# Kernel optimization log

Hardware: AMD Instinct MI355X
Metric: run time of the kernel (lower is better)

## Reference

```python
import jax, jax.numpy as jnp
import numpy as np

B, T, D, V, MEM = 2, 512, 512, 256, 256


def _gru(x, h0, wih, whh, bih, bhh):
    # x: [B,T,D], h0: [B,D]; torch GRU gate order: r, z, n
    def step(h, xt):
        gi = xt @ wih.T + bih            # [B,3D]
        gh = h @ whh.T + bhh             # [B,3D]
        i_r, i_z, i_n = jnp.split(gi, 3, axis=-1)
        h_r, h_z, h_n = jnp.split(gh, 3, axis=-1)
        r = jax.nn.sigmoid(i_r + h_r)
        z = jax.nn.sigmoid(i_z + h_z)
        n = jnp.tanh(i_n + r * h_n)
        h_new = (1.0 - z) * n + z * h
        return h_new, h_new
    hT, ys = jax.lax.scan(step, h0, jnp.swapaxes(x, 0, 1))
    return jnp.swapaxes(ys, 0, 1), hT


def _layernorm(x, g, b, eps=1e-5):
    m = jnp.mean(x, axis=-1, keepdims=True)
    v = jnp.mean((x - m) ** 2, axis=-1, keepdims=True)
    return (x - m) / jnp.sqrt(v + eps) * g + b


def setup_inputs() -> dict:
    key = jax.random.key(0)
    ks = jax.random.split(key, 24)
    s = 1.0 / np.sqrt(D)
    inp = {
        'x': jax.random.randint(ks[0], (B, T), 0, V, dtype=jnp.int32),
        'h_f': jnp.zeros((1, B, D), jnp.float32),
        'h_s': jnp.zeros((1, B, D), jnp.float32),
        'soma_w': jax.random.normal(ks[1], (V, D), jnp.float32),
        'fast_wih': jax.random.normal(ks[2], (3 * D, D)) * s,
        'fast_whh': jax.random.normal(ks[3], (3 * D, D)) * s,
        'fast_bih': jax.random.normal(ks[4], (3 * D,)) * s,
        'fast_bhh': jax.random.normal(ks[5], (3 * D,)) * s,
        'slow_wih': jax.random.normal(ks[6], (3 * D, D)) * s,
        'slow_whh': jax.random.normal(ks[7], (3 * D, D)) * s,
        'slow_bih': jax.random.normal(ks[8], (3 * D,)) * s,
        'slow_bhh': jax.random.normal(ks[9], (3 * D,)) * s,
        'qkv_w': jax.random.normal(ks[10], (3 * D, D)) * s,
        'qkv_b': jax.random.normal(ks[11], (3 * D,)) * s,
        'gate_w': jax.random.normal(ks[12], (D, D)) * s,
        'gate_b': jax.random.normal(ks[13], (D,)) * s,
        'gate_g': jnp.ones((D,), jnp.float32),
        'gate_bb': jnp.zeros((D,), jnp.float32),
        'mem_bank': jax.random.normal(ks[14], (MEM, D)) * 0.1,
        'hip_qw': jax.random.normal(ks[15], (D, D)) * s,
        'hip_qb': jax.random.normal(ks[16], (D,)) * s,
        'axon_w': jax.random.normal(ks[17], (D, 4 * D)) * (0.5 * s),
        'axon_b': jax.random.normal(ks[18], (D,)) * s,
        'norm_g': jnp.ones((D,), jnp.float32),
        'norm_b': jnp.zeros((D,), jnp.float32),
    }
    return inp


def reference(x, h_f, h_s, soma_w, fast_wih, fast_whh, fast_bih, fast_bhh,
              slow_wih, slow_whh, slow_bih, slow_bhh, qkv_w, qkv_b,
              gate_w, gate_b, gate_g, gate_bb, mem_bank, hip_qw, hip_qb,
              axon_w, axon_b, norm_g, norm_b):
    d = soma_w.shape[1]
    s_in = soma_w[x]  # mod[0] == 1.0
    p_f, hf1 = _gru(s_in, h_f[0], fast_wih, fast_whh, fast_bih, fast_bhh)
    p_s, hs1 = _gru(p_f, h_s[0], slow_wih, slow_whh, slow_bih, slow_bhh)
    # LinearIntentMemory: naive cumulative outer-product linear attention
    qkv = p_s @ qkv_w.T + qkv_b
    q, k, v = jnp.split(qkv, 3, axis=-1)
    q = jax.nn.elu(q) + 1.0
    k = jax.nn.elu(k) + 1.0
    kv_cum = jnp.cumsum(jnp.einsum('bti,btj->btij', k, v), axis=1)  # [B,T,D,D]
    num = jnp.einsum('bti,btij->btj', q, kv_cum)
    den = jnp.einsum('bti,bti->bt', q, jnp.cumsum(k, axis=1))[..., None] + 1e-6
    l_mem = num / den
    # intent gate: Linear -> LayerNorm -> Tanh
    intent = jnp.tanh(_layernorm(p_s @ gate_w.T + gate_b, gate_g, gate_bb))
    # hippocampus: softmax attention over memory bank
    qh = p_s @ hip_qw.T + hip_qb
    attn = qh @ mem_bank.T / jnp.sqrt(jnp.float32(d))
    episodes = jax.nn.softmax(attn, axis=-1) @ mem_bank
    combined = jnp.concatenate([p_f, intent, l_mem, episodes], axis=-1)
    thought = _layernorm(jnp.tanh(combined @ axon_w.T + axon_b), norm_g, norm_b)
    sw = soma_w / jnp.maximum(jnp.linalg.norm(soma_w, axis=-1, keepdims=True), 1e-12)
    logits = (thought @ sw.T) * 16.0
    return (logits, thought, hf1[None], hs1[None])
```

## Files before the change

### kernel.cpp

```cpp
#include <hip/hip_runtime.h>
#include <cstddef>

#define F_ELUQK 1
#define F_CAUSAL 2
#define F_DIV 4
#define F_NN 8
#define F_SCALE 16
#define FLAG_STRIDE 32
#define L_WGS 64
#define UNITS 8

enum : int {
  OFF_QH = 0,
  OFF_GI = 524288,
  OFF_COMB = OFF_GI + 1572864,
  OFF_PS = OFF_COMB + 2097152,
  OFF_QKV = OFF_PS + 524288,
  OFF_SCORES = OFF_QKV + 1572864,
  OFF_DEN = OFF_SCORES + 524288,
  OFF_TMP = OFF_DEN + 1024,
  OFF_ATTN = OFF_TMP + 524288,
  OFF_SW = OFF_ATTN + 262144,
  OFF_RING = OFF_SW + 131072,
  OFF_HSB = OFF_RING + 4096,
  OFF_FLAGS = OFF_HSB + 2048
};

__global__ __launch_bounds__(256) void gemm(
    const float* __restrict__ A, int lda, const float* __restrict__ B, int ldb,
    float* __restrict__ C, int ldc, int coff, int K,
    const float* __restrict__ bias, const float* __restrict__ den,
    float scale, int flags, int bBatch, const int* __restrict__ xidx) {
  __shared__ float As[16 * 65];
  __shared__ float Bs[16 * 65];
  int tid = threadIdx.x;
  int n0 = blockIdx.x * 64, m0 = blockIdx.y * 64;
  int rowoff = (m0 >> 9) * bBatch;
  int tx = tid & 15, ty = tid >> 4;

  if ((flags & F_CAUSAL) && n0 > ((m0 & 511) + 63)) {
    #pragma unroll
    for (int i = 0; i < 4; ++i)
      #pragma unroll
      for (int j = 0; j < 4; ++j)
        C[(size_t)(m0 + ty * 4 + i) * ldc + coff + n0 + tx * 4 + j] = 0.f;
    return;
  }

  float acc[4][4] = {};
  for (int k0 = 0; k0 < K; k0 += 16) {
    {
      int rr = tid >> 2, c4 = (tid & 3) << 2;
      int arow = m0 + rr;
      const float* ap = xidx ? (A + (size_t)xidx[arow] * 512 + (k0 + c4))
                             : (A + (size_t)arow * lda + (k0 + c4));
      float4 av = *(const float4*)ap;
      As[(c4 + 0) * 65 + rr] = av.x;
      As[(c4 + 1) * 65 + rr] = av.y;
      As[(c4 + 2) * 65 + rr] = av.z;
      As[(c4 + 3) * 65 + rr] = av.w;
    }
    if (!(flags & F_NN)) {
      int rr = tid >> 2, c4 = (tid & 3) << 2;
      const float* bp = B + (size_t)(n0 + rr + rowoff) * ldb + (k0 + c4);
      float4 bv = *(const float4*)bp;
      Bs[(c4 + 0) * 65 + rr] = bv.x; Bs[(c4 + 1) * 65 + rr] = bv.y;
      Bs[(c4 + 2) * 65 + rr] = bv.z; Bs[(c4 + 3) * 65 + rr] = bv.w;
    } else {
      int kk = tid >> 4, n4 = (tid & 15) << 2;
      const float* bp = B + (size_t)(k0 + kk + rowoff) * ldb + (n0 + n4);
      float4 bv = *(const float4*)bp;
      Bs[kk * 65 + n4 + 0] = bv.x; Bs[kk * 65 + n4 + 1] = bv.y;
      Bs[kk * 65 + n4 + 2] = bv.z; Bs[kk * 65 + n4 + 3] = bv.w;
    }
    __syncthreads();
    #pragma unroll
    for (int k = 0; k < 16; ++k) {
      float av[4], bv[4];
      #pragma unroll
      for (int i = 0; i < 4; ++i) av[i] = As[k * 65 + ty * 4 + i];
      #pragma unroll
      for (int j = 0; j < 4; ++j) bv[j] = Bs[k * 65 + tx * 4 + j];
      #pragma unroll
      for (int i = 0; i < 4; ++i)
        #pragma unroll
        for (int j = 0; j < 4; ++j)
          acc[i][j] = fmaf(av[i], bv[j], acc[i][j]);
    }
    __syncthreads();
  }
  #pragma unroll
  for (int i = 0; i < 4; ++i) {
    int m = m0 + ty * 4 + i;
    float dv = (flags & F_DIV) ? (1.0f / (den[m] + 1e-6f)) : 1.0f;
    #pragma unroll
    for (int j = 0; j < 4; ++j) {
      int n = n0 + tx * 4 + j;
      float v = acc[i][j];
      if (bias) v += bias[n];
      if (flags & F_ELUQK) { if (n < 1024) v = (v > 0.f) ? (v + 1.f) : __expf(v); }
      if (flags & F_CAUSAL) { if (n > (m & 511)) v = 0.f; }
      if (flags & F_SCALE) v *= scale;
      if (flags & F_DIV) v *= dv;
      C[(size_t)m * ldc + coff + n] = v;
    }
  }
}

__global__ __launch_bounds__(256) void gemm3(
    const float* __restrict__ A,
    const float* __restrict__ qkvw, const float* __restrict__ qkvb,
    const float* __restrict__ gatew, const float* __restrict__ gateb,
    const float* __restrict__ hipw, const float* __restrict__ hipb,
    float* __restrict__ QKV, float* __restrict__ TMP, float* __restrict__ QH) {
  __shared__ float As[16 * 65];
  __shared__ float Bs[16 * 65];
  int tid = threadIdx.x;
  int n0 = blockIdx.x * 64, m0 = blockIdx.y * 64;
  const float* B; const float* bias; float* C; int ldc, base;
  if (n0 < 1536) { B = qkvw; bias = qkvb; C = QKV; ldc = 1536; base = 0; }
  else if (n0 < 2048) { B = gatew; bias = gateb; C = TMP; ldc = 512; base = 1536; }
  else { B = hipw; bias = hipb; C = QH; ldc = 512; base = 2048; }
  int tx = tid & 15, ty = tid >> 4;
  float acc[4][4] = {};
  for (int k0 = 0; k0 < 512; k0 += 16) {
    {
      int rr = tid >> 2, c4 = (tid & 3) << 2;
      const float* ap = A + (size_t)(m0 + rr) * 512 + (k0 + c4);
      float4 av = *(const float4*)ap;
      As[(c4 + 0) * 65 + rr] = av.x; As[(c4 + 1) * 65 + rr] = av.y;
      As[(c4 + 2) * 65 + rr] = av.z; As[(c4 + 3) * 65 + rr] = av.w;
    }
    {
      int rr = tid >> 2, c4 = (tid & 3) << 2;
      const float* bp = B + (size_t)(n0 - base + rr) * 512 + (k0 + c4);
      float4 bv = *(const float4*)bp;
      Bs[(c4 + 0) * 65 + rr] = bv.x; Bs[(c4 + 1) * 65 + rr] = bv.y;
      Bs[(c4 + 2) * 65 + rr] = bv.z; Bs[(c4 + 3) * 65 + rr] = bv.w;
    }
    __syncthreads();
    #pragma unroll
    for (int k = 0; k < 16; ++k) {
      float av[4], bv[4];
      #pragma unroll
      for (int i = 0; i < 4; ++i) av[i] = As[k * 65 + ty * 4 + i];
      #pragma unroll
      for (int j = 0; j < 4; ++j) bv[j] = Bs[k * 65 + tx * 4 + j];
      #pragma unroll
      for (int i = 0; i < 4; ++i)
        #pragma unroll
        for (int j = 0; j < 4; ++j)
          acc[i][j] = fmaf(av[i], bv[j], acc[i][j]);
    }
    __syncthreads();
  }
  #pragma unroll
  for (int i = 0; i < 4; ++i) {
    int m = m0 + ty * 4 + i;
    #pragma unroll
    for (int j = 0; j < 4; ++j) {
      int n = n0 + tx * 4 + j;
      float v = acc[i][j] + bias[n - base];
      if (n < 1024) v = (v > 0.f) ? (v + 1.f) : __expf(v);
      C[(size_t)m * ldc + (n - base)] = v;
    }
  }
}

__device__ __forceinline__ void post_flag(unsigned* flags, int w, unsigned v) {
  __hip_atomic_store(flags + (size_t)w * FLAG_STRIDE, v, __ATOMIC_RELAXED,
                     __HIP_MEMORY_SCOPE_AGENT);
}
__device__ __forceinline__ void poll64(const unsigned* flags, unsigned tgt, int lane) {
  const unsigned* p = flags + (size_t)lane * FLAG_STRIDE;
  while (__hip_atomic_load(p, __ATOMIC_RELAXED, __HIP_MEMORY_SCOPE_AGENT) < tgt)
    __builtin_amdgcn_s_sleep(1);
}

__global__ __launch_bounds__(256, 1) void gru2_kernel(
    const float* __restrict__ gi,
    const float* __restrict__ fwhh, const float* __restrict__ fbhh,
    const float* __restrict__ h0f,
    const float* __restrict__ swih, const float* __restrict__ sbih,
    const float* __restrict__ swhh, const float* __restrict__ sbhh,
    const float* __restrict__ h0s,
    float* __restrict__ pf_out,
    float* __restrict__ ps_out,
    float* __restrict__ hfT, float* __restrict__ hsT,
    float* __restrict__ ring,
    float* __restrict__ hsbuf,
    unsigned* __restrict__ flagsA, unsigned* __restrict__ flagsB) {
  __shared__ __attribute__((aligned(16))) float hl[1024];
  __shared__ __attribute__((aligned(16))) float hfs[1024];
  __shared__ float P[48];
  __shared__ float Q[48];
  __shared__ float bl[24];
  __shared__ float bi[24];
  int tid = threadIdx.x, wg = blockIdx.x;
  bool L1 = wg < L_WGS;
  int j0 = (wg & (L_WGS - 1)) * UNITS;
  int part = tid & 7, r = tid >> 3;
  int g = r >> 3, u = r & 7;
  int wave = tid >> 6, lane = tid & 63;
  const float* whh = L1 ? fwhh : swhh;
  const float* bhh = L1 ? fbhh : sbhh;

  float4 wh[16], wi[16];
  if (r < 24) {
    const float* wp = whh + (size_t)(g * 512 + j0 + u) * 512 + part * 4;
    #pragma unroll
    for (int i = 0; i < 16; ++i) wh[i] = *(const float4*)(wp + i * 32);
    if (!L1) {
      const float* wp2 = swih + (size_t)(g * 512 + j0 + u) * 512 + part * 4;
      #pragma unroll
      for (int i = 0; i < 16; ++i) wi[i] = *(const float4*)(wp2 + i * 32);
    }
  }
  if (tid < 24) {
    bl[tid] = bhh[(tid >> 3) * 512 + j0 + (tid & 7)];
    if (!L1) bi[tid] = sbih[(tid >> 3) * 512 + j0 + (tid & 7)];
  }

  unsigned long long* hlq = (unsigned long long*)hl;
  unsigned long long* hfq = (unsigned long long*)hfs;
  const float4* h4 = (const float4*)hl;
  const float4* f4v = (const float4*)hfs;

  if (L1) {
    for (int t = 0; t < 512; ++t) {
      float i_r = 0.f, i_z = 0.f, i_n = 0.f;
      if (tid < 16) {
        int b = tid >> 3, jl = tid & 7;
        const float* girow = gi + (size_t)(b * 512 + t) * 1536 + j0 + jl;
        i_r = girow[0]; i_z = girow[512]; i_n = girow[1024];
      }
      if (wave == 0) {
        if (t > 0) poll64(flagsA, (unsigned)t, lane);
        unsigned long long v[8];
        if (t == 0) {
          const unsigned long long* s8 = (const unsigned long long*)h0f;
          #pragma unroll
          for (int k = 0; k < 8; ++k) v[k] = s8[k * 64 + lane];
        } else {
          const unsigned long long* s8 =
              (const unsigned long long*)(ring + ((t - 1) & 3) * 1024);
          #pragma unroll
          for (int k = 0; k < 8; ++k)
            v[k] = __hip_atomic_load(s8 + k * 64 + lane, __ATOMIC_RELAXED,
                                     __HIP_MEMORY_SCOPE_AGENT);
        }
        #pragma unroll
        for (int k = 0; k < 8; ++k) hlq[k * 64 + lane] = v[k];
      } else if (wave == 1) {
        if (t >= 4) poll64(flagsB, (unsigned)(t - 3), lane);
      }
      __syncthreads();
      if (r < 24) {
        float a0 = 0.f, a1 = 0.f;
        #pragma unroll
        for (int i = 0; i < 16; ++i) {
          float4 w = wh[i];
          float4 x0 = h4[i * 8 + part];
          float4 x1 = h4[128 + i * 8 + part];
          a0 += w.x * x0.x + w.y * x0.y + w.z * x0.z + w.w * x0.w;
          a1 += w.x * x1.x + w.y * x1.y + w.z * x1.z + w.w * x1.w;
        }
        a0 += __shfl_xor(a0, 1); a0 += __shfl_xor(a0, 2); a0 += __shfl_xor(a0, 4);
        a1 += __shfl_xor(a1, 1); a1 += __shfl_xor(a1, 2); a1 += __shfl_xor(a1, 4);
        if (part == 0) { P[r] = a0; P[24 + r] = a1; }
      }
      __syncthreads();
      if (tid < 16) {
        int b = tid >> 3, u2 = tid & 7, j = j0 + u2;
        float gh_r = P[b * 24 + u2] + bl[u2];
        float gh_z = P[b * 24 + 8 + u2] + bl[8 + u2];
        float gh_n = P[b * 24 + 16 + u2] + bl[16 + u2];
        float hold = hl[b * 512 + j];
        float rg = 1.0f / (1.0f + __expf(-(i_r + gh_r)));
        float zg = 1.0f / (1.0f + __expf(-(i_z + gh_z)));
        float ng = tanhf(i_n + rg * gh_n);
        float hnew = (1.0f - zg) * ng + zg * hold;
        __hip_atomic_store(ring + (size_t)(t & 3) * 1024 + b * 512 + j, hnew,
                           __ATOMIC_RELAXED, __HIP_MEMORY_SCOPE_AGENT);
        pf_out[(size_t)(b * 512 + t) * 2048 + j] = hnew;
        if (t == 511) hfT[b * 512 + j] = hnew;
      }
      __syncthreads();
      if (tid == 0) post_flag(flagsA, wg, (unsigned)(t + 1));
    }
  } else {
    for (int t2 = 0; t2 < 512; ++t2) {
      if (wave == 0) {
        poll64(flagsA, (unsigned)(t2 + 1), lane);
        const unsigned long long* f8 =
            (const unsigned long long*)(ring + (t2 & 3) * 1024);
        unsigned long long v[8];
        #pragma unroll
        for (int k = 0; k < 8; ++k)
          v[k] = __hip_atomic_load(f8 + k * 64 + lane, __ATOMIC_RELAXED,
                                   __HIP_MEMORY_SCOPE_AGENT);
        #pragma unroll
        for (int k = 0; k < 8; ++k) hfq[k * 64 + lane] = v[k];
      } else if (wave == 1) {
        unsigned long long v[8];
        if (t2 == 0) {
          const unsigned long long* s8 = (const unsigned long long*)h0s;
          #pragma unroll
          for (int k = 0; k < 8; ++k) v[k] = s8[k * 64 + lane];
        } else {
          poll64(flagsB, (unsigned)t2, lane);
          const unsigned long long* s8 =
              (const unsigned long long*)(hsbuf + ((t2 - 1) & 1) * 1024);
          #pragma unroll
          for (int k = 0; k < 8; ++k)
            v[k] = __hip_atomic_load(s8 + k * 64 + lane, __ATOMIC_RELAXED,
                                     __HIP_MEMORY_SCOPE_AGENT);
        }
        #pragma unroll
        for (int k = 0; k < 8; ++k) hlq[k * 64 + lane] = v[k];
      }
      __syncthreads();
      if (r < 24) {
        float a0 = 0.f, a1 = 0.f, c0 = 0.f, c1 = 0.f;
        #pragma unroll
        for (int i = 0; i < 16; ++i) {
          float4 w = wh[i];
          float4 x0 = h4[i * 8 + part];
          float4 x1 = h4[128 + i * 8 + part];
          a0 += w.x * x0.x + w.y * x0.y + w.z * x0.z + w.w * x0.w;
          a1 += w.x * x1.x + w.y * x1.y + w.z * x1.z + w.w * x1.w;
          float4 v = wi[i];
          float4 y0 = f4v[i * 8 + part];
          float4 y1 = f4v[128 + i * 8 + part];
          c0 += v.x * y0.x + v.y * y0.y + v.z * y0.z + v.w * y0.w;
          c1 += v.x * y1.x + v.y * y1.y + v.z * y1.z + v.w * y1.w;
        }
        a0 += __shfl_xor(a0, 1); a0 += __shfl_xor(a0, 2); a0 += __shfl_xor(a0, 4);
        a1 += __shfl_xor(a1, 1); a1 += __shfl_xor(a1, 2); a1 += __shfl_xor(a1, 4);
        c0 += __shfl_xor(c0, 1); c0 += __shfl_xor(c0, 2); c0 += __shfl_xor(c0, 4);
        c1 += __shfl_xor(c1, 1); c1 += __shfl_xor(c1, 2); c1 += __shfl_xor(c1, 4);
        if (part == 0) { P[r] = a0; P[24 + r] = a1; Q[r] = c0; Q[24 + r] = c1; }
      }
      __syncthreads();
      if (tid < 16) {
        int b = tid >> 3, u2 = tid & 7, j = j0 + u2;
        float i_r = Q[b * 24 + u2] + bi[u2];
        float i_z = Q[b * 24 + 8 + u2] + bi[8 + u2];
        float i_n = Q[b * 24 + 16 + u2] + bi[16 + u2];
        float gh_r = P[b * 24 + u2] + bl[u2];
        float gh_z = P[b * 24 + 8 + u2] + bl[8 + u2];
        float gh_n = P[b * 24 + 16 + u2] + bl[16 + u2];
        float hold = hl[b * 512 + j];
        float rg = 1.0f / (1.0f + __expf(-(i_r + gh_r)));
        float zg = 1.0f / (1.0f + __expf(-(i_z + gh_z)));
        float ng = tanhf(i_n + rg * gh_n);
        float hnew = (1.0f - zg) * ng + zg * hold;
        __hip_atomic_store(hsbuf + (size_t)(t2 & 1) * 1024 + b * 512 + j, hnew,
                           __ATOMIC_RELAXED, __HIP_MEMORY_SCOPE_AGENT);
        ps_out[(size_t)(b * 512 + t2) * 512 + j] = hnew;
        if (t2 == 511) hsT[b * 512 + j] = hnew;
      }
      __syncthreads();
      if (tid == 0) post_flag(flagsB, wg - L_WGS, (unsigned)(t2 + 1));
    }
  }
}

__global__ __launch_bounds__(256) void rowsum_kernel(const float* __restrict__ S,
                                                     float* __restrict__ den) {
  int m = blockIdx.x, tid = threadIdx.x;
  float s = S[(size_t)m * 512 + tid] + S[(size_t)m * 512 + 256 + tid];
  #pragma unroll
  for (int off = 32; off > 0; off >>= 1) s += __shfl_down(s, off);
  __shared__ float r4[4];
  if ((tid & 63) == 0) r4[tid >> 6] = s;
  __syncthreads();
  if (tid == 0) den[m] = r4[0] + r4[1] + r4[2] + r4[3];
}

__global__ __launch_bounds__(256) void softmax_kernel(float* __restrict__ a) {
  int m = blockIdx.x, tid = threadIdx.x;
  float v = a[(size_t)m * 256 + tid];
  float mx = v;
  #pragma unroll
  for (int off = 32; off > 0; off >>= 1) mx = fmaxf(mx, __shfl_down(mx, off));
  __shared__ float r4[4];
  __shared__ float s4[4];
  if ((tid & 63) == 0) r4[tid >> 6] = mx;
  __syncthreads();
  mx = fmaxf(fmaxf(r4[0], r4[1]), fmaxf(r4[2], r4[3]));
  float e = __expf(v - mx);
  float s = e;
  #pragma unroll
  for (int off = 32; off > 0; off >>= 1) s += __shfl_down(s, off);
  if ((tid & 63) == 0) s4[tid >> 6] = s;
  __syncthreads();
  s = s4[0] + s4[1] + s4[2] + s4[3];
  a[(size_t)m * 256 + tid] = e / s;
}

__global__ __launch_bounds__(256) void ln_kernel(
    const float* __restrict__ src, float* __restrict__ dst, int ldd, int dcoff,
    const float* __restrict__ gv, const float* __restrict__ bv, int tanhFirst) {
  int m = blockIdx.x, tid = threadIdx.x;
  float x0 = src[(size_t)m * 512 + tid];
  float x1 = src[(size_t)m * 512 + 256 + tid];
  if (tanhFirst) { x0 = tanhf(x0); x1 = tanhf(x1); }
  float s = x0 + x1, ss = x0 * x0 + x1 * x1;
  #pragma unroll
  for (int off = 32; off > 0; off >>= 1) { s += __shfl_down(s, off); ss += __shfl_down(ss, off); }
  __shared__ float rs[4], rss[4];
  if ((tid & 63) == 0) { rs[tid >> 6] = s; rss[tid >> 6] = ss; }
  __syncthreads();
  float st = rs[0] + rs[1] + rs[2] + rs[3];
  float sst = rss[0] + rss[1] + rss[2] + rss[3];
  float mean = st * (1.0f / 512.0f);
  float var = sst * (1.0f / 512.0f) - mean * mean;
  float inv = rsqrtf(var + 1e-5f);
  float y0 = (x0 - mean) * inv * gv[tid] + bv[tid];
  float y1 = (x1 - mean) * inv * gv[256 + tid] + bv[256 + tid];
  if (!tanhFirst) { y0 = tanhf(y0); y1 = tanhf(y1); }
  dst[(size_t)m * ldd + dcoff + tid] = y0;
  dst[(size_t)m * ldd + dcoff + 256 + tid] = y1;
}

__global__ __launch_bounds__(256) void swnorm_kernel(const float* __restrict__ soma,
                                                     float* __restrict__ sw) {
  int r = blockIdx.x, tid = threadIdx.x;
  float x0 = soma[(size_t)r * 512 + tid];
  float x1 = soma[(size_t)r * 512 + 256 + tid];
  float ss = x0 * x0 + x1 * x1;
  #pragma unroll
  for (int off = 32; off > 0; off >>= 1) ss += __shfl_down(ss, off);
  __shared__ float r4[4];
  if ((tid & 63) == 0) r4[tid >> 6] = ss;
  __syncthreads();
  float norm = sqrtf(r4[0] + r4[1] + r4[2] + r4[3]);
  norm = fmaxf(norm, 1e-12f);
  float inv = 1.0f / norm;
  sw[(size_t)r * 512 + tid] = x0 * inv;
  sw[(size_t)r * 512 + 256 + tid] = x1 * inv;
}

extern "C" void kernel_launch(void* const* d_in, const int* in_sizes, int n_in,
                              void* d_out, int out_size, void* d_ws, size_t ws_size,
                              hipStream_t stream) {
  (void)in_sizes; (void)n_in; (void)out_size; (void)ws_size;
  float* W = (float*)d_ws;
  float* outf = (float*)d_out;
  const int* x = (const int*)d_in[0];
  const float* soma = (const float*)d_in[3];

  hipMemsetAsync((char*)d_ws + (size_t)OFF_FLAGS * 4, 0, 16384, stream);

  gemm<<<dim3(24, 16), 256, 0, stream>>>(soma, 512, (const float*)d_in[4], 512,
      W + OFF_GI, 1536, 0, 512, (const float*)d_in[6], nullptr, 1.f, 0, 0, x);

  gru2_kernel<<<2 * L_WGS, 256, 0, stream>>>(W + OFF_GI,
      (const float*)d_in[5], (const float*)d_in[7], (const float*)d_in[1],
      (const float*)d_in[8], (const float*)d_in[10],
      (const float*)d_in[9], (const float*)d_in[11], (const float*)d_in[2],
      W + OFF_COMB, W + OFF_PS, outf + 786432, outf + 787456,
      W + OFF_RING, W + OFF_HSB,
      (unsigned*)(W + OFF_FLAGS), (unsigned*)(W + OFF_FLAGS) + L_WGS * FLAG_STRIDE);

  gemm3<<<dim3(40, 16), 256, 0, stream>>>(W + OFF_PS,
      (const float*)d_in[12], (const float*)d_in[13],
      (const float*)d_in[14], (const float*)d_in[15],
      (const float*)d_in[19], (const float*)d_in[20],
      W + OFF_QKV, W + OFF_TMP, W + OFF_QH);

  gemm<<<dim3(8, 16), 256, 0, stream>>>(W + OFF_QKV, 1536, W + OFF_QKV + 512, 1536,
      W + OFF_SCORES, 512, 0, 512, nullptr, nullptr, 1.f, F_CAUSAL, 512, nullptr);

  rowsum_kernel<<<1024, 256, 0, stream>>>(W + OFF_SCORES, W + OFF_DEN);

  gemm<<<dim3(8, 16), 256, 0, stream>>>(W + OFF_SCORES, 512, W + OFF_QKV + 1024, 1536,
      W + OFF_COMB, 2048, 1024, 512, nullptr, W + OFF_DEN, 1.f, F_NN | F_DIV, 512, nullptr);

  ln_kernel<<<1024, 256, 0, stream>>>(W + OFF_TMP, W + OFF_COMB, 2048, 512,
      (const float*)d_in[16], (const float*)d_in[17], 0);

  gemm<<<dim3(4, 16), 256, 0, stream>>>(W + OFF_QH, 512, (const float*)d_in[18], 512,
      W + OFF_ATTN, 256, 0, 512, nullptr, nullptr, 0.04419417382415922f, F_SCALE, 0, nullptr);
  softmax_kernel<<<1024, 256, 0, stream>>>(W + OFF_ATTN);
  gemm<<<dim3(8, 16), 256, 0, stream>>>(W + OFF_ATTN, 256, (const float*)d_in[18], 512,
      W + OFF_COMB, 2048, 1536, 256, nullptr, nullptr, 1.f, F_NN, 0, nullptr);

  gemm<<<dim3(8, 16), 256, 0, stream>>>(W + OFF_COMB, 2048, (const float*)d_in[21], 2048,
      W + OFF_TMP, 512, 0, 2048, (const float*)d_in[22], nullptr, 1.f, 0, 0, nullptr);
  ln_kernel<<<1024, 256, 0, stream>>>(W + OFF_TMP, outf + 262144, 512, 0,
      (const float*)d_in[23], (const float*)d_in[24], 1);

  swnorm_kernel<<<256, 256, 0, stream>>>(soma, W + OFF_SW);
  gemm<<<dim3(4, 16), 256, 0, stream>>>(outf + 262144, 512, W + OFF_SW, 512,
      outf, 256, 0, 512, nullptr, nullptr, 16.f, F_SCALE, 0, nullptr);
}
```

Baseline: 2.082 ms.

## Replace GRU step flags with sequence-tagged packed hidden-state words

Each hidden-state value is now written as a 64-bit word that packs the float with its step number. Consumers spin on the data itself across two waves instead of polling a separate per-workgroup flag array and then loading. This removes the layer-1 flag post and one barrier per step, and the layer-2 flag is now posted right after staging rather than after the gate update. The cost is twice the ring traffic and per-word polling loops, and correctness now depends on stale tags never matching the wanted step.

```diff
diff --git a/kernel.cpp b/kernel.cpp
--- a/kernel.cpp
+++ b/kernel.cpp
@@ -22,8 +22,8 @@
   OFF_ATTN = OFF_TMP + 524288,
   OFF_SW = OFF_ATTN + 262144,
   OFF_RING = OFF_SW + 131072,
-  OFF_HSB = OFF_RING + 4096,
-  OFF_FLAGS = OFF_HSB + 2048
+  OFF_HSB = OFF_RING + 8192,
+  OFF_FLAGS = OFF_HSB + 4096
 };
 
 __global__ __launch_bounds__(256) void gemm(
@@ -176,6 +176,28 @@
   while (__hip_atomic_load(p, __ATOMIC_RELAXED, __HIP_MEMORY_SCOPE_AGENT) < tgt)
     __builtin_amdgcn_s_sleep(1);
 }
+__device__ __forceinline__ void stage8(const unsigned long long* __restrict__ src,
+                                       float* __restrict__ dst,
+                                       unsigned want, int lane, int kbase) {
+  unsigned long long v[8];
+  unsigned need = 0xffu;
+  while (need) {
+    #pragma unroll
+    for (int k = 0; k < 8; ++k)
+      if (need >> k & 1)
+        v[k] = __hip_atomic_load(src + (size_t)(kbase + k) * 64 + lane,
+                                 __ATOMIC_RELAXED, __HIP_MEMORY_SCOPE_AGENT);
+    unsigned nn = 0;
+    #pragma unroll
+    for (int k = 0; k < 8; ++k)
+      if ((need >> k & 1) && (unsigned)(v[k] >> 32) != want) nn |= 1u << k;
+    if (nn) __builtin_amdgcn_s_sleep(1);
+    need = nn;
+  }
+  #pragma unroll
+  for (int k = 0; k < 8; ++k)
+    dst[(kbase + k) * 64 + lane] = __uint_as_float((unsigned)v[k]);
+}
 
 __global__ __launch_bounds__(256, 1) void gru2_kernel(
     const float* __restrict__ gi,
@@ -187,9 +209,9 @@
     float* __restrict__ pf_out,
     float* __restrict__ ps_out,
     float* __restrict__ hfT, float* __restrict__ hsT,
-    float* __restrict__ ring,
-    float* __restrict__ hsbuf,
-    unsigned* __restrict__ flagsA, unsigned* __restrict__ flagsB) {
+    unsigned long long* __restrict__ ringq,
+    unsigned long long* __restrict__ hsq,
+    unsigned* __restrict__ flagsB) {
   __shared__ __attribute__((aligned(16))) float hl[1024];
   __shared__ __attribute__((aligned(16))) float hfs[1024];
   __shared__ float P[48];
@@ -221,8 +243,6 @@
     if (!L1) bi[tid] = sbih[(tid >> 3) * 512 + j0 + (tid & 7)];
   }
 
-  unsigned long long* hlq = (unsigned long long*)hl;
-  unsigned long long* hfq = (unsigned long long*)hfs;
   const float4* h4 = (const float4*)hl;
   const float4* f4v = (const float4*)hfs;
 
@@ -234,26 +254,18 @@
         const float* girow = gi + (size_t)(b * 512 + t) * 1536 + j0 + jl;
         i_r = girow[0]; i_z = girow[512]; i_n = girow[1024];
       }
-      if (wave == 0) {
-        if (t > 0) poll64(flagsA, (unsigned)t, lane);
-        unsigned long long v[8];
-        if (t == 0) {
-          const unsigned long long* s8 = (const unsigned long long*)h0f;
-          #pragma unroll
-          for (int k = 0; k < 8; ++k) v[k] = s8[k * 64 + lane];
-        } else {
-          const unsigned long long* s8 =
-              (const unsigned long long*)(ring + ((t - 1) & 3) * 1024);
+      if (t == 0) {
+        if (wave < 2) {
           #pragma unroll
           for (int k = 0; k < 8; ++k)
-            v[k] = __hip_atomic_load(s8 + k * 64 + lane, __ATOMIC_RELAXED,
-                                     __HIP_MEMORY_SCOPE_AGENT);
+            hl[(wave * 8 + k) * 64 + lane] = h0f[(wave * 8 + k) * 64 + lane];
         }
-        #pragma unroll
-        for (int k = 0; k < 8; ++k) hlq[k * 64 + lane] = v[k];
-      } else if (wave == 1) {
-        if (t >= 4) poll64(flagsB, (unsigned)(t - 3), lane);
-      }
+      } else {
+        const unsigned long long* src = ringq + (size_t)((t - 1) & 3) * 1024;
+        if (wave == 0) stage8(src, hl, (unsigned)t, lane, 0);
+        else if (wave == 1) stage8(src, hl, (unsigned)t, lane, 8);
+      }
+      if (wave == 2 && t >= 4) poll64(flagsB, (unsigned)(t - 3), lane);
       __syncthreads();
       if (r < 24) {
         float a0 = 0.f, a1 = 0.f;
@@ -269,57 +281,44 @@
         a1 += __shfl_xor(a1, 1); a1 += __shfl_xor(a1, 2); a1 += __shfl_xor(a1, 4);
         if (part == 0) { P[r] = a0; P[24 + r] = a1; }
       }
+      float hold = 0.f;
+      if (tid < 16) hold = hl[(tid >> 3) * 512 + j0 + (tid & 7)];
       __syncthreads();
       if (tid < 16) {
         int b = tid >> 3, u2 = tid & 7, j = j0 + u2;
         float gh_r = P[b * 24 + u2] + bl[u2];
         float gh_z = P[b * 24 + 8 + u2] + bl[8 + u2];
         float gh_n = P[b * 24 + 16 + u2] + bl[16 + u2];
-        float hold = hl[b * 512 + j];
         float rg = 1.0f / (1.0f + __expf(-(i_r + gh_r)));
         float zg = 1.0f / (1.0f + __expf(-(i_z + gh_z)));
         float ng = tanhf(i_n + rg * gh_n);
         float hnew = (1.0f - zg) * ng + zg * hold;
-        __hip_atomic_store(ring + (size_t)(t & 3) * 1024 + b * 512 + j, hnew,
+        unsigned long long pk = ((unsigned long long)(unsigned)(t + 1) << 32) |
+                                (unsigned long long)__float_as_uint(hnew);
+        __hip_atomic_store(ringq + (size_t)(t & 3) * 1024 + b * 512 + j, pk,
                            __ATOMIC_RELAXED, __HIP_MEMORY_SCOPE_AGENT);
         pf_out[(size_t)(b * 512 + t) * 2048 + j] = hnew;
         if (t == 511) hfT[b * 512 + j] = hnew;
       }
-      __syncthreads();
-      if (tid == 0) post_flag(flagsA, wg, (unsigned)(t + 1));
     }
   } else {
     for (int t2 = 0; t2 < 512; ++t2) {
-      if (wave == 0) {
-        poll64(flagsA, (unsigned)(t2 + 1), lane);
-        const unsigned long long* f8 =
-            (const unsigned long long*)(ring + (t2 & 3) * 1024);
-        unsigned long long v[8];
-        #pragma unroll
-        for (int k = 0; k < 8; ++k)
-          v[k] = __hip_atomic_load(f8 + k * 64 + lane, __ATOMIC_RELAXED,
-                                   __HIP_MEMORY_SCOPE_AGENT);
-        #pragma unroll
-        for (int k = 0; k < 8; ++k) hfq[k * 64 + lane] = v[k];
-      } else if (wave == 1) {
-        unsigned long long v[8];
-        if (t2 == 0) {
-          const unsigned long long* s8 = (const unsigned long long*)h0s;
-          #pragma unroll
-          for (int k = 0; k < 8; ++k) v[k] = s8[k * 64 + lane];
-        } else {
-          poll64(flagsB, (unsigned)t2, lane);
-          const unsigned long long* s8 =
-              (const unsigned long long*)(hsbuf + ((t2 - 1) & 1) * 1024);
+      {
+        const unsigned long long* src = ringq + (size_t)(t2 & 3) * 1024;
+        if (wave == 0) stage8(src, hfs, (unsigned)(t2 + 1), lane, 0);
+        else if (wave == 1) stage8(src, hfs, (unsigned)(t2 + 1), lane, 8);
+        else if (t2 == 0) {
           #pragma unroll
           for (int k = 0; k < 8; ++k)
-            v[k] = __hip_atomic_load(s8 + k * 64 + lane, __ATOMIC_RELAXED,
-                                     __HIP_MEMORY_SCOPE_AGENT);
+            hl[((wave - 2) * 8 + k) * 64 + lane] = h0s[((wave - 2) * 8 + k) * 64 + lane];
+        } else {
+          const unsigned long long* s2 = hsq + (size_t)((t2 - 1) & 1) * 1024;
+          if (wave == 2) stage8(s2, hl, (unsigned)t2, lane, 0);
+          else stage8(s2, hl, (unsigned)t2, lane, 8);
         }
-        #pragma unroll
-        for (int k = 0; k < 8; ++k) hlq[k * 64 + lane] = v[k];
       }
       __syncthreads();
+      if (tid == 0) post_flag(flagsB, wg - L_WGS, (unsigned)(t2 + 1));
       if (r < 24) {
         float a0 = 0.f, a1 = 0.f, c0 = 0.f, c1 = 0.f;
         #pragma unroll
@@ -341,6 +340,8 @@
         c1 += __shfl_xor(c1, 1); c1 += __shfl_xor(c1, 2); c1 += __shfl_xor(c1, 4);
         if (part == 0) { P[r] = a0; P[24 + r] = a1; Q[r] = c0; Q[24 + r] = c1; }
       }
+      float hold = 0.f;
+      if (tid < 16) hold = hl[(tid >> 3) * 512 + j0 + (tid & 7)];
       __syncthreads();
       if (tid < 16) {
         int b = tid >> 3, u2 = tid & 7, j = j0 + u2;
@@ -350,18 +351,17 @@
         float gh_r = P[b * 24 + u2] + bl[u2];
         float gh_z = P[b * 24 + 8 + u2] + bl[8 + u2];
         float gh_n = P[b * 24 + 16 + u2] + bl[16 + u2];
-        float hold = hl[b * 512 + j];
         float rg = 1.0f / (1.0f + __expf(-(i_r + gh_r)));
         float zg = 1.0f / (1.0f + __expf(-(i_z + gh_z)));
         float ng = tanhf(i_n + rg * gh_n);
         float hnew = (1.0f - zg) * ng + zg * hold;
-        __hip_atomic_store(hsbuf + (size_t)(t2 & 1) * 1024 + b * 512 + j, hnew,
+        unsigned long long pk = ((unsigned long long)(unsigned)(t2 + 1) << 32) |
+                                (unsigned long long)__float_as_uint(hnew);
+        __hip_atomic_store(hsq + (size_t)(t2 & 1) * 1024 + b * 512 + j, pk,
                            __ATOMIC_RELAXED, __HIP_MEMORY_SCOPE_AGENT);
         ps_out[(size_t)(b * 512 + t2) * 512 + j] = hnew;
         if (t2 == 511) hsT[b * 512 + j] = hnew;
       }
-      __syncthreads();
-      if (tid == 0) post_flag(flagsB, wg - L_WGS, (unsigned)(t2 + 1));
     }
   }
 }
@@ -451,7 +451,7 @@
   const int* x = (const int*)d_in[0];
   const float* soma = (const float*)d_in[3];
 
-  hipMemsetAsync((char*)d_ws + (size_t)OFF_FLAGS * 4, 0, 16384, stream);
+  hipMemsetAsync((char*)d_ws + (size_t)OFF_FLAGS * 4, 0, 8192, stream);
 
   gemm<<<dim3(24, 16), 256, 0, stream>>>(soma, 512, (const float*)d_in[4], 512,
       W + OFF_GI, 1536, 0, 512, (const float*)d_in[6], nullptr, 1.f, 0, 0, x);
@@ -461,8 +461,8 @@
       (const float*)d_in[8], (const float*)d_in[10],
       (const float*)d_in[9], (const float*)d_in[11], (const float*)d_in[2],
       W + OFF_COMB, W + OFF_PS, outf + 786432, outf + 787456,
-      W + OFF_RING, W + OFF_HSB,
-      (unsigned*)(W + OFF_FLAGS), (unsigned*)(W + OFF_FLAGS) + L_WGS * FLAG_STRIDE);
+      (unsigned long long*)(W + OFF_RING), (unsigned long long*)(W + OFF_HSB),
+      (unsigned*)(W + OFF_FLAGS));
 
   gemm3<<<dim3(40, 16), 256, 0, stream>>>(W + OFF_PS,
       (const float*)d_in[12], (const float*)d_in[13],
```

Measured after the change: 2.187 ms. +5.1%, slower.
